# Kernel tuning notes

Measured on AMD Instinct MI355X. Metric: run time of the kernel, lower is better.

## Reference

```python
import jax, jax.numpy as jnp
import numpy as np

N_LAYERS = 4
D_MODEL = 1024
D_INNER = 2048
DT_RANK = 64
D_STATE = 16
D_CONV = 4
EPS = 1e-5


def _rms(x, w):
    return x * jax.lax.rsqrt(jnp.mean(x * x, axis=-1, keepdims=True) + EPS) * w


def _silu(x):
    return x * jax.nn.sigmoid(x)


def setup_inputs() -> dict:
    key = jax.random.key(0)
    ks = jax.random.split(key, 8)
    B, L = 2, 1024
    s = 0.02
    nl, dm, di = N_LAYERS, D_MODEL, D_INNER
    return {
        "x": jax.random.normal(ks[0], (B, L, dm), dtype=jnp.float32),
        "norm_w": jnp.ones((nl, dm), dtype=jnp.float32),
        "W_in": jax.random.normal(ks[1], (nl, 2 * di, dm), dtype=jnp.float32) * s,
        "conv_w": jax.random.normal(ks[2], (nl, di, D_CONV), dtype=jnp.float32) * s,
        "conv_b": jnp.zeros((nl, di), dtype=jnp.float32),
        "W_x": jax.random.normal(ks[3], (nl, DT_RANK + 2 * D_STATE, di), dtype=jnp.float32) * s,
        "W_dt": jax.random.normal(ks[4], (nl, di, DT_RANK), dtype=jnp.float32) * (DT_RANK ** -0.5),
        "b_dt": jax.random.normal(ks[5], (nl, di), dtype=jnp.float32) - 3.0,  # softplus -> small dt, like inv-softplus init
        "A_log": jax.random.uniform(ks[6], (nl, di, D_STATE), dtype=jnp.float32) * 2.0,  # A = -exp(A_log) in [-7.4, -1]
        "D": jnp.ones((nl, di), dtype=jnp.float32),
        "W_out": jax.random.normal(ks[7], (nl, dm, di), dtype=jnp.float32) * s,
    }


def reference(x, norm_w, W_in, conv_w, conv_b, W_x, W_dt, b_dt, A_log, D, W_out):
    nl = W_in.shape[0]
    L = x.shape[1]
    dc = conv_w.shape[-1]
    n = A_log.shape[-1]
    rk = W_dt.shape[-1]

    def combine(left, right):
        a1, b1 = left
        a2, b2 = right
        return a2 * a1, a2 * b1 + b2

    for i in range(nl):
        h = _rms(x, norm_w[i])
        xz = jnp.einsum('bld,ed->ble', h, W_in[i])          # [B,L,2*Di]
        xi, z = jnp.split(xz, 2, axis=-1)
        # causal depthwise conv1d (padding=dc-1, keep first L outputs)
        xp = jnp.pad(xi, ((0, 0), (dc - 1, 0), (0, 0)))
        xc = conv_b[i] + sum(xp[:, k:k + L, :] * conv_w[i][:, k] for k in range(dc))
        xc = _silu(xc)
        # SSM parameterization
        dbc = jnp.einsum('bld,ed->ble', xc, W_x[i])          # [B,L,rk+2n]
        delta, Bm, Cm = jnp.split(dbc, [rk, rk + n], axis=-1)
        delta = jax.nn.softplus(jnp.einsum('blr,dr->bld', delta, W_dt[i]) + b_dt[i])  # [B,L,Di]
        A = -jnp.exp(A_log[i])                               # [Di,N]
        deltaA = jnp.exp(delta[..., None] * A)               # [B,L,Di,N]
        BX = (delta * xc)[..., None] * Bm[:, :, None, :]     # [B,L,Di,N]
        # parallel scan: h_t = deltaA_t * h_{t-1} + BX_t
        _, hs = jax.lax.associative_scan(combine, (deltaA, BX), axis=1)
        y = jnp.einsum('bldn,bln->bld', hs, Cm) + D[i] * xc
        out = jnp.einsum('bld,ed->ble', y * _silu(z), W_out[i])
        x = x + out
    return x
```

## Files before the change

kernel.cpp:

```cpp
#include <hip/hip_runtime.h>
#include <hip/hip_bf16.h>
#include <math.h>

#define NL 4
#define DM 1024
#define DI 2048
#define RK 64
#define NS 16
#define LSEQ 1024
#define BATCH 2
#define MROWS (BATCH*LSEQ)
#define NCHUNK 32
#define LC 32

typedef __attribute__((ext_vector_type(8))) short bf16x8;
typedef __attribute__((ext_vector_type(4))) float f32x4;

__device__ __forceinline__ float bf2f(unsigned short u){
  union { unsigned int i; float f; } v; v.i = ((unsigned int)u) << 16; return v.f;
}
__device__ __forceinline__ unsigned short f2bf(float f){
  union { float f; unsigned int i; } v; v.f = f;
  unsigned int r = v.i + 0x7fffu + ((v.i >> 16) & 1u);
  return (unsigned short)(r >> 16);
}
__device__ __forceinline__ float sigmoidf_(float x){ return 1.0f / (1.0f + __expf(-x)); }
__device__ __forceinline__ float softplusf_(float x){ return (x > 20.0f) ? x : log1pf(__expf(x)); }

__device__ __forceinline__ void gl2lds16(const void* g, void* l) {
  __builtin_amdgcn_global_load_lds((__attribute__((address_space(1))) void*)g,
                                   (__attribute__((address_space(3))) void*)l,
                                   16, 0, 0);
}

template<int BM, int BN, int WAVES_M, int WAVES_N, int EPI>
__global__ __launch_bounds__(256)
void gemm_bt(const unsigned short* __restrict__ A, const unsigned short* __restrict__ W,
             void* __restrict__ C, const float* __restrict__ bias,
             int M, int N, int K, int ldc, int kslices)
{
  constexpr int MT = BM / (WAVES_M * 16);
  constexpr int NT = BN / (WAVES_N * 16);
  __shared__ __align__(16) unsigned short As[BM * 64];
  __shared__ __align__(16) unsigned short Bs[BN * 64];

  const int tid  = threadIdx.x;
  const int wave = tid >> 6;
  const int lane = tid & 63;
  const int wm   = wave / WAVES_N;
  const int wn   = wave % WAVES_N;
  const int quad = lane >> 4;
  const int l16  = lane & 15;
  const int srow = lane >> 3;
  const int scol = ((lane & 7) ^ srow) * 8;

  const int m0 = blockIdx.x * BM;
  const int n0 = blockIdx.y * BN;
  const int Ks = K / kslices;
  const int kb = blockIdx.z * Ks;

  f32x4 acc[MT][NT];
  #pragma unroll
  for (int i = 0; i < MT; i++)
    #pragma unroll
    for (int j = 0; j < NT; j++)
      acc[i][j] = (f32x4){0.f, 0.f, 0.f, 0.f};

  for (int k0 = kb; k0 < kb + Ks; k0 += 64) {
    const unsigned short* Ab = A + (size_t)m0 * K + k0;
    #pragma unroll
    for (int i = 0; i < BM / 32; i++) {
      int c = i * 4 + wave;
      gl2lds16(Ab + (size_t)(c * 8 + srow) * K + scol, As + c * 512);
    }
    const unsigned short* Wb = W + (size_t)n0 * K + k0;
    #pragma unroll
    for (int i = 0; i < BN / 32; i++) {
      int c = i * 4 + wave;
      gl2lds16(Wb + (size_t)(c * 8 + srow) * K + scol, Bs + c * 512);
    }
    __syncthreads();

    #pragma unroll
    for (int h = 0; h < 2; h++) {
      bf16x8 af[MT], bfr[NT];
      #pragma unroll
      for (int mt = 0; mt < MT; mt++) {
        int rA = wm * MT * 16 + mt * 16 + l16;
        af[mt] = *(const bf16x8*)(As + rA * 64 + (((h * 4 + quad) ^ (rA & 7)) << 3));
      }
      #pragma unroll
      for (int nt = 0; nt < NT; nt++) {
        int rB = wn * NT * 16 + nt * 16 + l16;
        bfr[nt] = *(const bf16x8*)(Bs + rB * 64 + (((h * 4 + quad) ^ (rB & 7)) << 3));
      }
      #pragma unroll
      for (int mt = 0; mt < MT; mt++)
        #pragma unroll
        for (int nt = 0; nt < NT; nt++)
          acc[mt][nt] = __builtin_amdgcn_mfma_f32_16x16x32_bf16(af[mt], bfr[nt], acc[mt][nt], 0, 0, 0);
    }
    __syncthreads();
  }

  const size_t slice_off = (size_t)blockIdx.z * M * ldc;
  #pragma unroll
  for (int mt = 0; mt < MT; mt++) {
    #pragma unroll
    for (int nt = 0; nt < NT; nt++) {
      int n = n0 + wn * NT * 16 + nt * 16 + l16;
      #pragma unroll
      for (int r = 0; r < 4; r++) {
        int m = m0 + wm * MT * 16 + mt * 16 + quad * 4 + r;
        float v = acc[mt][nt][r];
        size_t off = (size_t)m * ldc + n;
        if constexpr (EPI == 0)      ((unsigned short*)C)[off] = f2bf(v);
        else                         ((float*)C)[slice_off + off] = v;
      }
    }
  }
}

#define G3R 8
#define G3C 256
#define G3P 264
__global__ __launch_bounds__(256)
void gemm3_fused(const float* __restrict__ dbc, const unsigned short* __restrict__ Wdt,
                 const float* __restrict__ b_dt, float* __restrict__ delta)
{
  __shared__ float dts[G3R][RK];
  __shared__ __align__(16) unsigned short Ws[RK][G3P];
  const int tid = threadIdx.x;
  const int m0 = blockIdx.x * G3R;
  const int c0 = blockIdx.y * G3C;

  {
    int r = tid >> 5, k = (tid & 31) * 2;
    float2 v = *(const float2*)(dbc + (size_t)(m0 + r) * 96 + k);
    dts[r][k] = v.x; dts[r][k + 1] = v.y;
  }
  {
    const unsigned short* wrow = Wdt + (size_t)(c0 + tid) * RK;
    #pragma unroll
    for (int ch = 0; ch < 8; ch++) {
      union { bf16x8 v; unsigned short u[8]; } w;
      w.v = *(const bf16x8*)(wrow + ch * 8);
      #pragma unroll
      for (int j = 0; j < 8; j++) Ws[ch * 8 + j][tid] = w.u[j];
    }
  }
  __syncthreads();

  const int r  = tid >> 5;
  const int cg = tid & 31;
  float acc[8] = {0.f, 0.f, 0.f, 0.f, 0.f, 0.f, 0.f, 0.f};
  #pragma unroll 4
  for (int k = 0; k < RK; k++) {
    float a = dts[r][k];
    union { bf16x8 v; unsigned short u[8]; } w;
    w.v = *(const bf16x8*)&Ws[k][cg * 8];
    #pragma unroll
    for (int j = 0; j < 8; j++) acc[j] += a * bf2f(w.u[j]);
  }

  const int m = m0 + r, c = c0 + cg * 8;
  float4 b0 = *(const float4*)(b_dt + c);
  float4 b1 = *(const float4*)(b_dt + c + 4);
  float bb[8] = {b0.x, b0.y, b0.z, b0.w, b1.x, b1.y, b1.z, b1.w};
  float out[8];
  #pragma unroll
  for (int j = 0; j < 8; j++) {
    float v = acc[j] + bb[j];
    out[j] = (v > 15.0f) ? v : __logf(1.0f + __expf(v));
  }
  float* dp = delta + (size_t)m * DI + c;
  *(float4*)dp       = (float4){out[0], out[1], out[2], out[3]};
  *(float4*)(dp + 4) = (float4){out[4], out[5], out[6], out[7]};
}

__global__ __launch_bounds__(256)
void reduce4_kernel(const float* __restrict__ part, float* __restrict__ x)
{
  const size_t MN = (size_t)MROWS * DM;
  int i = blockIdx.x * 256 + threadIdx.x;
  float4 a = ((const float4*)part)[i];
  float4 b = ((const float4*)(part + MN))[i];
  float4 c = ((const float4*)(part + 2 * MN))[i];
  float4 d = ((const float4*)(part + 3 * MN))[i];
  float4 o = ((float4*)x)[i];
  o.x += a.x + b.x + c.x + d.x;
  o.y += a.y + b.y + c.y + d.y;
  o.z += a.z + b.z + c.z + d.z;
  o.w += a.w + b.w + c.w + d.w;
  ((float4*)x)[i] = o;
}

__global__ __launch_bounds__(256)
void reduce2_kernel(const float* __restrict__ part, float* __restrict__ dbc)
{
  const int MN = MROWS * 96;
  int i = blockIdx.x * 256 + threadIdx.x;
  dbc[i] = part[i] + part[MN + i] + part[2 * MN + i] + part[3 * MN + i];
}

__global__ __launch_bounds__(256)
void rmsnorm_kernel(const float* __restrict__ x, const float* __restrict__ w,
                    unsigned short* __restrict__ h)
{
  const int row = blockIdx.x;
  const float4 a = ((const float4*)(x + (size_t)row * DM))[threadIdx.x];
  float ss = a.x*a.x + a.y*a.y + a.z*a.z + a.w*a.w;
  #pragma unroll
  for (int o = 32; o > 0; o >>= 1) ss += __shfl_down(ss, o);
  __shared__ float red[4];
  if ((threadIdx.x & 63) == 0) red[threadIdx.x >> 6] = ss;
  __syncthreads();
  float rs = rsqrtf((red[0] + red[1] + red[2] + red[3]) * (1.0f / DM) + 1e-5f);
  const float4 wv = ((const float4*)w)[threadIdx.x];
  ushort4 o4;
  o4.x = f2bf(a.x * rs * wv.x);
  o4.y = f2bf(a.y * rs * wv.y);
  o4.z = f2bf(a.z * rs * wv.z);
  o4.w = f2bf(a.w * rs * wv.w);
  ((ushort4*)(h + (size_t)row * DM))[threadIdx.x] = o4;
}

__global__ __launch_bounds__(256)
void conv_silu_kernel(const unsigned short* __restrict__ xz,
                      const float* __restrict__ cw, const float* __restrict__ cb,
                      unsigned short* __restrict__ xc)
{
  int idx = blockIdx.x * 256 + threadIdx.x;
  int d = idx & (DI - 1);
  int t = (idx >> 11) & (LSEQ - 1);
  int b = idx >> 21;
  const float4 w4 = ((const float4*)cw)[d];
  const float wk[4] = {w4.x, w4.y, w4.z, w4.w};
  const unsigned short* xi = xz + (size_t)b * LSEQ * (2 * DI) + d;
  float acc = cb[d];
  #pragma unroll
  for (int k = 0; k < 4; k++) {
    int tt = t - 3 + k;
    if (tt >= 0) acc += bf2f(xi[(size_t)tt * (2 * DI)]) * wk[k];
  }
  xc[idx] = f2bf(acc * sigmoidf_(acc));
}

__global__ void convert_all_kernel(const float* __restrict__ W_in, unsigned short* __restrict__ Win_bf,
                                   const float* __restrict__ W_x,  unsigned short* __restrict__ Wx_bf,
                                   const float* __restrict__ W_dt, unsigned short* __restrict__ Wdt_bf,
                                   const float* __restrict__ W_out,unsigned short* __restrict__ Wout_bf)
{
  const float* src[4]  = {W_in, W_x, W_dt, W_out};
  unsigned short* dst[4] = {Win_bf, Wx_bf, Wdt_bf, Wout_bf};
  const int n4[4] = {NL*2*DI*DM/4, NL*96*DI/4, NL*DI*RK/4, NL*DM*DI/4};
  for (int s = 0; s < 4; s++) {
    int stride = gridDim.x * 256;
    for (int i = blockIdx.x * 256 + threadIdx.x; i < n4[s]; i += stride) {
      float4 v = ((const float4*)src[s])[i];
      ushort4 o; o.x = f2bf(v.x); o.y = f2bf(v.y); o.z = f2bf(v.z); o.w = f2bf(v.w);
      ((ushort4*)dst[s])[i] = o;
    }
  }
}

__global__ __launch_bounds__(256)
void scan1_kernel(const float* __restrict__ delta, const unsigned short* __restrict__ xc,
                  const float* __restrict__ dbc, const float* __restrict__ A_log,
                  float* __restrict__ hend, float* __restrict__ sumd)
{
  const int d = blockIdx.x * 256 + threadIdx.x;
  const int c = blockIdx.y;
  const int b = blockIdx.z;
  const int t0 = c * LC;
  __shared__ float bc[LC][32];
  #pragma unroll
  for (int i = 0; i < (LC * 32) / 256; i++) {
    int f = i * 256 + threadIdx.x;
    int r = f >> 5, col = f & 31;
    bc[r][col] = dbc[(size_t)(b * LSEQ + t0 + r) * 96 + 64 + col];
  }
  float Av[NS], h[NS];
  #pragma unroll
  for (int n = 0; n < NS; n++) { Av[n] = -__expf(A_log[(size_t)d * NS + n]); h[n] = 0.f; }
  __syncthreads();
  float sd = 0.f;
  for (int t = 0; t < LC; t++) {
    size_t ix = (size_t)(b * LSEQ + t0 + t) * DI + d;
    float dt = delta[ix];
    float xcv = bf2f(xc[ix]);
    sd += dt;
    float dx = dt * xcv;
    #pragma unroll
    for (int n = 0; n < NS; n++) {
      float da = __expf(dt * Av[n]);
      h[n] = da * h[n] + dx * bc[t][n];
    }
  }
  size_t base = ((size_t)(b * NCHUNK + c) * NS) * DI + d;
  #pragma unroll
  for (int n = 0; n < NS; n++) hend[base + (size_t)n * DI] = h[n];
  sumd[(size_t)(b * NCHUNK + c) * DI + d] = sd;
}

__global__ __launch_bounds__(256)
void scan2_kernel(const float* __restrict__ A_log, const float* __restrict__ hend,
                  const float* __restrict__ sumd, float* __restrict__ hin)
{
  int g = blockIdx.x * 256 + threadIdx.x;
  int b = g >> 11;
  int d = g & (DI - 1);
  float Av[NS], H[NS];
  #pragma unroll
  for (int n = 0; n < NS; n++) { Av[n] = -__expf(A_log[(size_t)d * NS + n]); H[n] = 0.f; }
  for (int c = 0; c < NCHUNK; c++) {
    size_t base = ((size_t)(b * NCHUNK + c) * NS) * DI + d;
    float sd = sumd[(size_t)(b * NCHUNK + c) * DI + d];
    #pragma unroll
    for (int n = 0; n < NS; n++) {
      hin[base + (size_t)n * DI] = H[n];
      float da = __expf(Av[n] * sd);
      H[n] = da * H[n] + hend[base + (size_t)n * DI];
    }
  }
}

__global__ __launch_bounds__(256)
void scan3_kernel(const float* __restrict__ delta, const unsigned short* __restrict__ xc,
                  const float* __restrict__ dbc, const float* __restrict__ A_log,
                  const float* __restrict__ hin, const float* __restrict__ Dvec,
                  const unsigned short* __restrict__ xz, unsigned short* __restrict__ g)
{
  const int d = blockIdx.x * 256 + threadIdx.x;
  const int c = blockIdx.y;
  const int b = blockIdx.z;
  const int t0 = c * LC;
  __shared__ float bc[LC][32];
  #pragma unroll
  for (int i = 0; i < (LC * 32) / 256; i++) {
    int f = i * 256 + threadIdx.x;
    int r = f >> 5, col = f & 31;
    bc[r][col] = dbc[(size_t)(b * LSEQ + t0 + r) * 96 + 64 + col];
  }
  float Av[NS], h[NS];
  size_t base = ((size_t)(b * NCHUNK + c) * NS) * DI + d;
  #pragma unroll
  for (int n = 0; n < NS; n++) {
    Av[n] = -__expf(A_log[(size_t)d * NS + n]);
    h[n] = hin[base + (size_t)n * DI];
  }
  const float Dd = Dvec[d];
  __syncthreads();
  for (int t = 0; t < LC; t++) {
    size_t ix = (size_t)(b * LSEQ + t0 + t) * DI + d;
    float dt = delta[ix];
    float xcv = bf2f(xc[ix]);
    float dx = dt * xcv;
    float y = Dd * xcv;
    #pragma unroll
    for (int n = 0; n < NS; n++) {
      float da = __expf(dt * Av[n]);
      h[n] = da * h[n] + dx * bc[t][n];
      y += h[n] * bc[t][16 + n];
    }
    float zv = bf2f(xz[(size_t)(b * LSEQ + t0 + t) * (2 * DI) + DI + d]);
    g[ix] = f2bf(y * (zv * sigmoidf_(zv)));
  }
}

extern "C" void kernel_launch(void* const* d_in, const int* in_sizes, int n_in,
                              void* d_out, int out_size, void* d_ws, size_t ws_size,
                              hipStream_t stream)
{
  const float* x_in   = (const float*)d_in[0];
  const float* norm_w = (const float*)d_in[1];
  const float* W_in   = (const float*)d_in[2];
  const float* conv_w = (const float*)d_in[3];
  const float* conv_b = (const float*)d_in[4];
  const float* W_x    = (const float*)d_in[5];
  const float* W_dt   = (const float*)d_in[6];
  const float* b_dt   = (const float*)d_in[7];
  const float* A_log  = (const float*)d_in[8];
  const float* Dv     = (const float*)d_in[9];
  const float* W_out  = (const float*)d_in[10];
  float* x = (float*)d_out;

  char* p = (char*)d_ws;
  auto alloc = [&](size_t bytes) {
    void* r = (void*)p;
    p += (bytes + 255) & ~(size_t)255;
    return r;
  };
  unsigned short* Win_bf  = (unsigned short*)alloc((size_t)NL * 2 * DI * DM * 2);
  unsigned short* Wx_bf   = (unsigned short*)alloc((size_t)NL * 96 * DI * 2);
  unsigned short* Wdt_bf  = (unsigned short*)alloc((size_t)NL * DI * RK * 2);
  unsigned short* Wout_bf = (unsigned short*)alloc((size_t)NL * DM * DI * 2);
  unsigned short* h_bf    = (unsigned short*)alloc((size_t)MROWS * DM * 2);
  unsigned short* xz_bf   = (unsigned short*)alloc((size_t)MROWS * 2 * DI * 2);
  unsigned short* xc_bf   = (unsigned short*)alloc((size_t)MROWS * DI * 2);
  float*          dbc     = (float*)alloc((size_t)MROWS * 96 * 4);
  unsigned short* g_bf    = (unsigned short*)alloc((size_t)MROWS * DI * 2);
  float*          delta   = (float*)alloc((size_t)MROWS * DI * 4);
  float*          hend    = (float*)alloc((size_t)BATCH * NCHUNK * NS * DI * 4);
  float*          hin     = (float*)alloc((size_t)BATCH * NCHUNK * NS * DI * 4);
  float*          sumd    = (float*)alloc((size_t)BATCH * NCHUNK * DI * 4);
  float* part2 = delta;
  float* part4 = delta;

  hipMemcpyAsync(x, x_in, (size_t)MROWS * DM * 4, hipMemcpyDeviceToDevice, stream);

  convert_all_kernel<<<2048, 256, 0, stream>>>(W_in, Win_bf, W_x, Wx_bf,
                                               W_dt, Wdt_bf, W_out, Wout_bf);

  for (int l = 0; l < NL; l++) {
    const unsigned short* Win_l  = Win_bf  + (size_t)l * 2 * DI * DM;
    const unsigned short* Wx_l   = Wx_bf   + (size_t)l * 96 * DI;
    const unsigned short* Wdt_l  = Wdt_bf  + (size_t)l * DI * RK;
    const unsigned short* Wout_l = Wout_bf + (size_t)l * DM * DI;

    rmsnorm_kernel<<<MROWS, 256, 0, stream>>>(x, norm_w + (size_t)l * DM, h_bf);

    gemm_bt<128, 128, 2, 2, 0><<<dim3(MROWS / 128, (2 * DI) / 128), 256, 0, stream>>>(
        h_bf, Win_l, xz_bf, nullptr, MROWS, 2 * DI, DM, 2 * DI, 1);

    conv_silu_kernel<<<(BATCH * LSEQ * DI) / 256, 256, 0, stream>>>(
        xz_bf, conv_w + (size_t)l * DI * 4, conv_b + (size_t)l * DI, xc_bf);

    gemm_bt<64, 96, 4, 1, 4><<<dim3(MROWS / 64, 1, 4), 256, 0, stream>>>(
        xc_bf, Wx_l, part2, nullptr, MROWS, 96, DI, 96, 4);
    reduce2_kernel<<<(MROWS * 96) / 256, 256, 0, stream>>>(part2, dbc);

    gemm3_fused<<<dim3(MROWS / G3R, DI / G3C), 256, 0, stream>>>(
        dbc, Wdt_l, b_dt + (size_t)l * DI, delta);

    scan1_kernel<<<dim3(DI / 256, NCHUNK, BATCH), 256, 0, stream>>>(
        delta, xc_bf, dbc, A_log + (size_t)l * DI * NS, hend, sumd);
    scan2_kernel<<<(BATCH * DI) / 256, 256, 0, stream>>>(
        A_log + (size_t)l * DI * NS, hend, sumd, hin);
    scan3_kernel<<<dim3(DI / 256, NCHUNK, BATCH), 256, 0, stream>>>(
        delta, xc_bf, dbc, A_log + (size_t)l * DI * NS, hin, Dv + (size_t)l * DI, xz_bf, g_bf);

    gemm_bt<128, 128, 2, 2, 4><<<dim3(MROWS / 128, DM / 128, 4), 256, 0, stream>>>(
        g_bf, Wout_l, part4, nullptr, MROWS, DM, DI, DM, 4);
    reduce4_kernel<<<(MROWS * DM) / 1024, 256, 0, stream>>>(part4, x);
  }
}
```

Baseline: 851.5 us.

## Store delta in bf16, retune GEMM tiles and split-K, vectorize weight conversion

The softplus output delta is now written as bf16 instead of fp32, which halves its write traffic in gemm3 and its read traffic in both scan passes. The in-projection and out-projection GEMMs move to 64x128 tiles, and the out-projection drops from 4 to 2 split-K slices, so its reduction reads fewer partial buffers. Split-K partials now reuse the hend/hin scratch space instead of the delta buffer. The weight conversion kernel becomes one flat loop with 8-wide loads, and the unused bias argument is removed. Rounding delta to bf16 adds error to the exponent term of the scan.

```diff
diff --git a/kernel.cpp b/kernel.cpp
--- a/kernel.cpp
+++ b/kernel.cpp
@@ -25,7 +25,6 @@
   return (unsigned short)(r >> 16);
 }
 __device__ __forceinline__ float sigmoidf_(float x){ return 1.0f / (1.0f + __expf(-x)); }
-__device__ __forceinline__ float softplusf_(float x){ return (x > 20.0f) ? x : log1pf(__expf(x)); }
 
 __device__ __forceinline__ void gl2lds16(const void* g, void* l) {
   __builtin_amdgcn_global_load_lds((__attribute__((address_space(1))) void*)g,
@@ -36,8 +35,7 @@
 template<int BM, int BN, int WAVES_M, int WAVES_N, int EPI>
 __global__ __launch_bounds__(256)
 void gemm_bt(const unsigned short* __restrict__ A, const unsigned short* __restrict__ W,
-             void* __restrict__ C, const float* __restrict__ bias,
-             int M, int N, int K, int ldc, int kslices)
+             void* __restrict__ C, int M, int N, int K, int ldc, int kslices)
 {
   constexpr int MT = BM / (WAVES_M * 16);
   constexpr int NT = BN / (WAVES_N * 16);
@@ -126,7 +124,7 @@
 #define G3P 264
 __global__ __launch_bounds__(256)
 void gemm3_fused(const float* __restrict__ dbc, const unsigned short* __restrict__ Wdt,
-                 const float* __restrict__ b_dt, float* __restrict__ delta)
+                 const float* __restrict__ b_dt, unsigned short* __restrict__ delta)
 {
   __shared__ float dts[G3R][RK];
   __shared__ __align__(16) unsigned short Ws[RK][G3P];
@@ -167,15 +165,13 @@
   float4 b0 = *(const float4*)(b_dt + c);
   float4 b1 = *(const float4*)(b_dt + c + 4);
   float bb[8] = {b0.x, b0.y, b0.z, b0.w, b1.x, b1.y, b1.z, b1.w};
-  float out[8];
+  union { unsigned short u[8]; uint4 v; } o;
   #pragma unroll
   for (int j = 0; j < 8; j++) {
     float v = acc[j] + bb[j];
-    out[j] = (v > 15.0f) ? v : __logf(1.0f + __expf(v));
-  }
-  float* dp = delta + (size_t)m * DI + c;
-  *(float4*)dp       = (float4){out[0], out[1], out[2], out[3]};
-  *(float4*)(dp + 4) = (float4){out[4], out[5], out[6], out[7]};
+    o.u[j] = f2bf((v > 15.0f) ? v : __logf(1.0f + __expf(v)));
+  }
+  *(uint4*)(delta + (size_t)m * DI + c) = o.v;
 }
 
 __global__ __launch_bounds__(256)
@@ -185,13 +181,11 @@
   int i = blockIdx.x * 256 + threadIdx.x;
   float4 a = ((const float4*)part)[i];
   float4 b = ((const float4*)(part + MN))[i];
-  float4 c = ((const float4*)(part + 2 * MN))[i];
-  float4 d = ((const float4*)(part + 3 * MN))[i];
   float4 o = ((float4*)x)[i];
-  o.x += a.x + b.x + c.x + d.x;
-  o.y += a.y + b.y + c.y + d.y;
-  o.z += a.z + b.z + c.z + d.z;
-  o.w += a.w + b.w + c.w + d.w;
+  o.x += a.x + b.x;
+  o.y += a.y + b.y;
+  o.z += a.z + b.z;
+  o.w += a.w + b.w;
   ((float4*)x)[i] = o;
 }
 
@@ -246,26 +240,35 @@
   xc[idx] = f2bf(acc * sigmoidf_(acc));
 }
 
+#define SEG0 (NL*2*DI*DM)
+#define SEG1 (SEG0 + NL*96*DI)
+#define SEG2 (SEG1 + NL*DI*RK)
+#define SEG3 (SEG2 + NL*DM*DI)
 __global__ void convert_all_kernel(const float* __restrict__ W_in, unsigned short* __restrict__ Win_bf,
                                    const float* __restrict__ W_x,  unsigned short* __restrict__ Wx_bf,
                                    const float* __restrict__ W_dt, unsigned short* __restrict__ Wdt_bf,
                                    const float* __restrict__ W_out,unsigned short* __restrict__ Wout_bf)
 {
-  const float* src[4]  = {W_in, W_x, W_dt, W_out};
-  unsigned short* dst[4] = {Win_bf, Wx_bf, Wdt_bf, Wout_bf};
-  const int n4[4] = {NL*2*DI*DM/4, NL*96*DI/4, NL*DI*RK/4, NL*DM*DI/4};
-  for (int s = 0; s < 4; s++) {
-    int stride = gridDim.x * 256;
-    for (int i = blockIdx.x * 256 + threadIdx.x; i < n4[s]; i += stride) {
-      float4 v = ((const float4*)src[s])[i];
-      ushort4 o; o.x = f2bf(v.x); o.y = f2bf(v.y); o.z = f2bf(v.z); o.w = f2bf(v.w);
-      ((ushort4*)dst[s])[i] = o;
-    }
-  }
-}
-
-__global__ __launch_bounds__(256)
-void scan1_kernel(const float* __restrict__ delta, const unsigned short* __restrict__ xc,
+  const int T8 = SEG3 / 8;
+  int stride = gridDim.x * 256;
+  for (int i = blockIdx.x * 256 + threadIdx.x; i < T8; i += stride) {
+    int e = i * 8;
+    const float* s; unsigned short* d; int off;
+    if (e < SEG0)      { s = W_in;  d = Win_bf;  off = e; }
+    else if (e < SEG1) { s = W_x;   d = Wx_bf;   off = e - SEG0; }
+    else if (e < SEG2) { s = W_dt;  d = Wdt_bf;  off = e - SEG1; }
+    else               { s = W_out; d = Wout_bf; off = e - SEG2; }
+    float4 a = *(const float4*)(s + off);
+    float4 b = *(const float4*)(s + off + 4);
+    union { unsigned short u[8]; uint4 v; } o;
+    o.u[0] = f2bf(a.x); o.u[1] = f2bf(a.y); o.u[2] = f2bf(a.z); o.u[3] = f2bf(a.w);
+    o.u[4] = f2bf(b.x); o.u[5] = f2bf(b.y); o.u[6] = f2bf(b.z); o.u[7] = f2bf(b.w);
+    *(uint4*)(d + off) = o.v;
+  }
+}
+
+__global__ __launch_bounds__(256)
+void scan1_kernel(const unsigned short* __restrict__ delta, const unsigned short* __restrict__ xc,
                   const float* __restrict__ dbc, const float* __restrict__ A_log,
                   float* __restrict__ hend, float* __restrict__ sumd)
 {
@@ -287,7 +290,7 @@
   float sd = 0.f;
   for (int t = 0; t < LC; t++) {
     size_t ix = (size_t)(b * LSEQ + t0 + t) * DI + d;
-    float dt = delta[ix];
+    float dt = bf2f(delta[ix]);
     float xcv = bf2f(xc[ix]);
     sd += dt;
     float dx = dt * xcv;
@@ -326,7 +329,7 @@
 }
 
 __global__ __launch_bounds__(256)
-void scan3_kernel(const float* __restrict__ delta, const unsigned short* __restrict__ xc,
+void scan3_kernel(const unsigned short* __restrict__ delta, const unsigned short* __restrict__ xc,
                   const float* __restrict__ dbc, const float* __restrict__ A_log,
                   const float* __restrict__ hin, const float* __restrict__ Dvec,
                   const unsigned short* __restrict__ xz, unsigned short* __restrict__ g)
@@ -353,7 +356,7 @@
   __syncthreads();
   for (int t = 0; t < LC; t++) {
     size_t ix = (size_t)(b * LSEQ + t0 + t) * DI + d;
-    float dt = delta[ix];
+    float dt = bf2f(delta[ix]);
     float xcv = bf2f(xc[ix]);
     float dx = dt * xcv;
     float y = Dd * xcv;
@@ -400,12 +403,12 @@
   unsigned short* xc_bf   = (unsigned short*)alloc((size_t)MROWS * DI * 2);
   float*          dbc     = (float*)alloc((size_t)MROWS * 96 * 4);
   unsigned short* g_bf    = (unsigned short*)alloc((size_t)MROWS * DI * 2);
-  float*          delta   = (float*)alloc((size_t)MROWS * DI * 4);
+  unsigned short* delta   = (unsigned short*)alloc((size_t)MROWS * DI * 2);
   float*          hend    = (float*)alloc((size_t)BATCH * NCHUNK * NS * DI * 4);
   float*          hin     = (float*)alloc((size_t)BATCH * NCHUNK * NS * DI * 4);
   float*          sumd    = (float*)alloc((size_t)BATCH * NCHUNK * DI * 4);
-  float* part2 = delta;
-  float* part4 = delta;
+  float* part2 = hend;
+  float* part4 = hend;
 
   hipMemcpyAsync(x, x_in, (size_t)MROWS * DM * 4, hipMemcpyDeviceToDevice, stream);
 
@@ -420,14 +423,14 @@
 
     rmsnorm_kernel<<<MROWS, 256, 0, stream>>>(x, norm_w + (size_t)l * DM, h_bf);
 
-    gemm_bt<128, 128, 2, 2, 0><<<dim3(MROWS / 128, (2 * DI) / 128), 256, 0, stream>>>(
-        h_bf, Win_l, xz_bf, nullptr, MROWS, 2 * DI, DM, 2 * DI, 1);
+    gemm_bt<64, 128, 2, 2, 0><<<dim3(MROWS / 64, (2 * DI) / 128), 256, 0, stream>>>(
+        h_bf, Win_l, xz_bf, MROWS, 2 * DI, DM, 2 * DI, 1);
 
     conv_silu_kernel<<<(BATCH * LSEQ * DI) / 256, 256, 0, stream>>>(
         xz_bf, conv_w + (size_t)l * DI * 4, conv_b + (size_t)l * DI, xc_bf);
 
     gemm_bt<64, 96, 4, 1, 4><<<dim3(MROWS / 64, 1, 4), 256, 0, stream>>>(
-        xc_bf, Wx_l, part2, nullptr, MROWS, 96, DI, 96, 4);
+        xc_bf, Wx_l, part2, MROWS, 96, DI, 96, 4);
     reduce2_kernel<<<(MROWS * 96) / 256, 256, 0, stream>>>(part2, dbc);
 
     gemm3_fused<<<dim3(MROWS / G3R, DI / G3C), 256, 0, stream>>>(
@@ -440,8 +443,8 @@
     scan3_kernel<<<dim3(DI / 256, NCHUNK, BATCH), 256, 0, stream>>>(
         delta, xc_bf, dbc, A_log + (size_t)l * DI * NS, hin, Dv + (size_t)l * DI, xz_bf, g_bf);
 
-    gemm_bt<128, 128, 2, 2, 4><<<dim3(MROWS / 128, DM / 128, 4), 256, 0, stream>>>(
-        g_bf, Wout_l, part4, nullptr, MROWS, DM, DI, DM, 4);
+    gemm_bt<64, 128, 2, 2, 4><<<dim3(MROWS / 64, DM / 128, 2), 256, 0, stream>>>(
+        g_bf, Wout_l, part4, MROWS, DM, DI, DM, 2);
     reduce4_kernel<<<(MROWS * DM) / 1024, 256, 0, stream>>>(part4, x);
   }
 }
```

Result: no change. 844.4 us (-0.8%).
